# Kernel optimization log

Hardware: AMD Instinct MI355X
Metric: run time of the kernel (lower is better)

## Reference

```python
import jax, jax.numpy as jnp
import numpy as np

B, C_IN, C_OUT, H, W, W_DIM, K = 4, 64, 64, 512, 512, 512, 3
LRELU_SLOPE = 0.2
ACT_GAIN = np.sqrt(2.0).astype(np.float32)  # lrelu def_gain
CONV_CLAMP = 256.0


def setup_inputs() -> dict:
    key = jax.random.key(0)
    ks = jax.random.split(key, 5)
    return {
        "x": jax.random.normal(ks[0], (B, C_IN, H, W), dtype=jnp.float32),
        "ws": jax.random.normal(ks[1], (B, W_DIM), dtype=jnp.float32),
        "noise": jax.random.normal(ks[2], (B, 1, H, W), dtype=jnp.float32),
        "affine_weight": jax.random.normal(ks[3], (C_IN, W_DIM), dtype=jnp.float32),
        "affine_bias": jnp.ones((C_IN,), dtype=jnp.float32),
        "conv_weight": jax.random.normal(ks[4], (C_OUT, C_IN, K, K), dtype=jnp.float32),
        "bias": jnp.zeros((C_OUT,), dtype=jnp.float32),
    }


def reference(x, ws, noise, affine_weight, affine_bias, conv_weight, bias):
    b, c_in, h, w_sp = x.shape
    c_out, _, kh, kw = conv_weight.shape
    w_dim = ws.shape[1]

    # Affine (FullyConnectedLayer with equalized LR: weight_gain = 1/sqrt(w_dim), bias_init=1)
    styles = ws @ (affine_weight.T * np.float32(1.0 / np.sqrt(w_dim))) + affine_bias  # [b, c_in]

    # Modulate per-sample weights: w = weight[None] * styles
    wmod = conv_weight[None] * styles[:, None, :, None, None]  # [b, c_out, c_in, kh, kw]

    # Demodulation coefficients
    demod = jax.lax.rsqrt(jnp.sum(jnp.square(wmod), axis=(2, 3, 4)) + 1e-8)  # [b, c_out]
    wmod = wmod * demod[:, :, None, None, None]

    # Fused grouped conv: groups = batch (conv2d_resample, up=down=1, flip_weight=True -> correlation)
    xg = x.reshape(1, b * c_in, h, w_sp)
    wg = wmod.reshape(b * c_out, c_in, kh, kw)
    pad = kh // 2
    y = jax.lax.conv_general_dilated(
        xg, wg, window_strides=(1, 1), padding=[(pad, pad), (pad, pad)],
        dimension_numbers=("NCHW", "OIHW", "NCHW"), feature_group_count=b)
    y = y.reshape(b, c_out, h, w_sp)

    # Noise add (broadcast over channels)
    y = y + noise

    # bias_act: bias + lrelu * act_gain, then clamp (conv_clamp * gain, gain=1)
    y = y + bias[None, :, None, None]
    y = jnp.where(y >= 0, y, LRELU_SLOPE * y) * ACT_GAIN
    y = jnp.clip(y, -CONV_CLAMP, CONV_CLAMP)
    return y
```

## Files before the change

kernel.cpp:

```cpp
#include <hip/hip_runtime.h>
#include <math.h>

#define HH 512
#define WW 512
#define HW (HH * WW)
#define PW 514
#define PPIX (PW * PW)

typedef short bf16x8 __attribute__((ext_vector_type(8)));
typedef float f32x4 __attribute__((ext_vector_type(4)));

__device__ __forceinline__ ushort f2bf(float f) {
    union { float f; uint u; } c; c.f = f;
    uint u = c.u;
    return (ushort)((u + 0x7fffu + ((u >> 16) & 1u)) >> 16);
}

__device__ __forceinline__ uint cvtpk(float a, float b) {
    uint r;
    asm("v_cvt_pk_bf16_f32 %0, %1, %2" : "=v"(r) : "v"(a), "v"(b));
    return r;
}

__global__ void k_styles(const float* __restrict__ wsv, const float* __restrict__ aw,
                         const float* __restrict__ ab, float* __restrict__ styles) {
    int bid = blockIdx.x;
    int b = bid >> 6, ci = bid & 63;
    int l = threadIdx.x;
    const float* wrow = wsv + b * 512;
    const float* arow = aw + ci * 512;
    float s = 0.f;
    #pragma unroll
    for (int j = 0; j < 8; ++j)
        s += wrow[l + 64 * j] * arow[l + 64 * j];
    #pragma unroll
    for (int off = 32; off; off >>= 1)
        s += __shfl_xor(s, off, 64);
    if (l == 0)
        styles[b * 64 + ci] = s * 0.044194173824159216f + ab[ci];
}

__global__ void k_wmod(const float* __restrict__ cw, const float* __restrict__ styles,
                       ushort* __restrict__ wb) {
    int b = blockIdx.x >> 6, co = blockIdx.x & 63;
    int ci = threadIdx.x;
    float st = styles[b * 64 + ci];
    const float* wp = cw + (co * 64 + ci) * 9;
    float wv[9];
    float ss = 0.f;
    #pragma unroll
    for (int k = 0; k < 9; ++k) { wv[k] = wp[k] * st; ss += wv[k] * wv[k]; }
    #pragma unroll
    for (int off = 32; off; off >>= 1)
        ss += __shfl_xor(ss, off, 64);
    float dm = 1.0f / sqrtf(ss + 1e-8f);
    int cisw = ((((ci >> 3) ^ co) & 7) << 3) | (ci & 7);
    #pragma unroll
    for (int k = 0; k < 9; ++k)
        wb[((size_t)(b * 64 + co) * 9 + k) * 64 + cisw] = f2bf(wv[k] * dm);
}

__global__ void k_zeropad(ushort* __restrict__ xp) {
    int id = blockIdx.x * 256 + threadIdx.x;
    if (id >= 4 * 2052) return;
    int b = id / 2052, r = id % 2052;
    int gyp, gxp;
    if (r < 514)       { gyp = 0;        gxp = r; }
    else if (r < 1028) { gyp = 513;      gxp = r - 514; }
    else if (r < 1540) { gyp = r - 1027; gxp = 0; }
    else               { gyp = r - 1539; gxp = 513; }
    ushort* p = xp + (((size_t)b * PW + gyp) * PW + gxp) * 64;
    uint4 z = make_uint4(0, 0, 0, 0);
    #pragma unroll
    for (int i = 0; i < 8; ++i) *(uint4*)(p + i * 8) = z;
}

__global__ __launch_bounds__(256) void k_xpose(
    const float* __restrict__ x, ushort* __restrict__ xp) {
    __shared__ ushort lt[128 * 68];
    const int t = threadIdx.x;
    const int bid = blockIdx.x;
    const int gxt = bid & 3;
    const int gy  = (bid >> 2) & 511;
    const int b   = bid >> 11;

    const float* xb = x + (size_t)b * 64 * HW + (size_t)gy * WW + gxt * 128;
    const int ci0 = 8 * (t >> 5);
    const int gxc = t & 31;

    f32x4 v[8];
    #pragma unroll
    for (int j = 0; j < 8; ++j)
        v[j] = *(const f32x4*)(xb + (size_t)(ci0 + j) * HW + gxc * 4);

    #pragma unroll
    for (int p = 0; p < 4; ++p) {
        int px = gxc * 4 + p;
        int rowp = ((px & 3) * 32 + (px >> 2)) * 68;
        #pragma unroll
        for (int cg = 0; cg < 2; ++cg) {
            uint lo = cvtpk(v[4 * cg + 0][p], v[4 * cg + 1][p]);
            uint hi = cvtpk(v[4 * cg + 2][p], v[4 * cg + 3][p]);
            *(uint2*)&lt[rowp + ci0 + 4 * cg] = make_uint2(lo, hi);
        }
    }
    __syncthreads();

    const int px = t >> 1, half = t & 1;
    const int rowp = ((px & 3) * 32 + (px >> 2)) * 68 + half * 32;
    uint4 o0 = *(uint4*)&lt[rowp + 0];
    uint4 o1 = *(uint4*)&lt[rowp + 8];
    uint4 o2 = *(uint4*)&lt[rowp + 16];
    uint4 o3 = *(uint4*)&lt[rowp + 24];
    ushort* dst = xp + (((size_t)b * PW + (gy + 1)) * PW + (gxt * 128 + px + 1)) * 64
                     + half * 32;
    *(uint4*)(dst + 0)  = o0;
    *(uint4*)(dst + 8)  = o1;
    *(uint4*)(dst + 16) = o2;
    *(uint4*)(dst + 24) = o3;
}

__global__ __launch_bounds__(256) void k_conv(
    const ushort* __restrict__ xp,
    const ushort* __restrict__ wb,
    const float* __restrict__ noise,
    const float* __restrict__ bias,
    float* __restrict__ out) {
    __shared__ ushort tileB[1472 * 8];
    __shared__ ushort wlds[32 * 9 * 64];

    const int t = threadIdx.x;
    const int b = blockIdx.y;
    const int coh = blockIdx.z;
    const int colb = blockIdx.x & 31;
    const int rowb = blockIdx.x >> 5;
    const int tx = colb * 16, ty = rowb * 8;
    const int w = t >> 6;
    const int lane = t & 63;

    const ushort* xpb = xp + (size_t)b * PPIX * 64;
    const ushort* wA  = wb + (size_t)(b * 64 + coh * 32) * 576;

    for (int j = w; j < 36; j += 4) {
        const ushort* src = wA + j * 512 + lane * 8;
        __builtin_amdgcn_global_load_lds(
            (const __attribute__((address_space(1))) unsigned int*)src,
            (__attribute__((address_space(3))) unsigned int*)&wlds[j * 512],
            16, 0, 0);
    }
    for (int j = w; j < 23; j += 4) {
        int c = j * 64 + lane;
        int c2 = c < 1439 ? c : 1439;
        int cig = c2 & 7;
        int pxl = c2 >> 3;
        int row = pxl / 18;
        int lcol = pxl - row * 18;
        int gsrc = cig ^ (lcol & 7);
        const ushort* src = xpb + ((size_t)(ty + row) * PW + (tx + lcol)) * 64 + gsrc * 8;
        __builtin_amdgcn_global_load_lds(
            (const __attribute__((address_space(1))) unsigned int*)src,
            (__attribute__((address_space(3))) unsigned int*)&tileB[j * 512],
            16, 0, 0);
    }
    asm volatile("s_waitcnt vmcnt(0)" ::: "memory");
    __syncthreads();

    const int lr = lane & 15;
    const int lq = lane >> 4;

    int aidx[2][2];
    #pragma unroll
    for (int mt = 0; mt < 2; ++mt)
        #pragma unroll
        for (int kb = 0; kb < 2; ++kb)
            aidx[mt][kb] = (mt * 16 + lr) * 576 + ((((kb << 2) | lq) ^ (lr & 7)) << 3);

    int bidx[2][3];
    #pragma unroll
    for (int i = 0; i < 2; ++i)
        #pragma unroll
        for (int dx = 0; dx < 3; ++dx) {
            int lcol = lr + dx;
            bidx[i][dx] = ((2 * w + i) * 18 + lcol) * 64 + ((lq * 8) ^ ((lcol & 7) << 3));
        }

    f32x4 acc[2][2];
    #pragma unroll
    for (int mt = 0; mt < 2; ++mt)
        #pragma unroll
        for (int i = 0; i < 2; ++i) acc[mt][i] = (f32x4){0.f, 0.f, 0.f, 0.f};

    #pragma unroll
    for (int dy = 0; dy < 3; ++dy) {
        #pragma unroll
        for (int dx = 0; dx < 3; ++dx) {
            #pragma unroll
            for (int kb = 0; kb < 2; ++kb) {
                const int off = dy * 3 + dx;
                bf16x8 afr[2], bfr[2];
                #pragma unroll
                for (int mt = 0; mt < 2; ++mt)
                    afr[mt] = *(const bf16x8*)&wlds[aidx[mt][kb] + off * 64];
                #pragma unroll
                for (int i = 0; i < 2; ++i) {
                    int idx = (bidx[i][dx] + dy * (18 * 64)) ^ (kb << 5);
                    bfr[i] = *(const bf16x8*)&tileB[idx];
                }
                #pragma unroll
                for (int mt = 0; mt < 2; ++mt)
                    #pragma unroll
                    for (int i = 0; i < 2; ++i)
                        acc[mt][i] = __builtin_amdgcn_mfma_f32_16x16x32_bf16(
                            afr[mt], bfr[i], acc[mt][i], 0, 0, 0);
            }
        }
    }

    const float* nz = noise + (size_t)b * HW;
    float nv[2];
    int gyv[2];
    const int gx = tx + lr;
    #pragma unroll
    for (int i = 0; i < 2; ++i) {
        gyv[i] = ty + 2 * w + i;
        nv[i] = nz[gyv[i] * WW + gx];
    }
    #pragma unroll
    for (int mt = 0; mt < 2; ++mt) {
        f32x4 bv = *(const f32x4*)&bias[coh * 32 + mt * 16 + lq * 4];
        #pragma unroll
        for (int i = 0; i < 2; ++i) {
            #pragma unroll
            for (int rg2 = 0; rg2 < 4; ++rg2) {
                int co = coh * 32 + mt * 16 + lq * 4 + rg2;
                float y = acc[mt][i][rg2] + nv[i] + bv[rg2];
                y = (y >= 0.f ? y : 0.2f * y) * 1.41421356237f;
                y = fminf(fmaxf(y, -256.f), 256.f);
                out[((size_t)(b * 64 + co) * HH + gyv[i]) * WW + gx] = y;
            }
        }
    }
}

extern "C" void kernel_launch(void* const* d_in, const int* in_sizes, int n_in,
                              void* d_out, int out_size, void* d_ws, size_t ws_size,
                              hipStream_t stream) {
    const float* x     = (const float*)d_in[0];
    const float* wsv   = (const float*)d_in[1];
    const float* noise = (const float*)d_in[2];
    const float* aw    = (const float*)d_in[3];
    const float* ab    = (const float*)d_in[4];
    const float* cw    = (const float*)d_in[5];
    const float* bias  = (const float*)d_in[6];
    float* out = (float*)d_out;

    float*  styles = (float*)d_ws;
    ushort* wb16   = (ushort*)((char*)d_ws + 1024);
    ushort* xpad   = (ushort*)((char*)d_ws + (1 << 20));

    k_styles<<<256, 64, 0, stream>>>(wsv, aw, ab, styles);
    k_wmod<<<256, 64, 0, stream>>>(cw, styles, wb16);
    k_zeropad<<<33, 256, 0, stream>>>(xpad);
    k_xpose<<<8192, 256, 0, stream>>>(x, xpad);
    dim3 grid(2048, 4, 2);
    k_conv<<<grid, 256, 0, stream>>>(xpad, wb16, noise, bias, out);
}
```

Baseline: 267.9 us.

## Make conv kernel persistent over 16 tiles with double-buffered input staging

The conv kernel now launches 512 blocks. Each block loads all 64 output channels' modulated weights into LDS once and loops over 16 spatial tiles. The next input tile is prefetched into a second LDS buffer with async global-to-LDS loads while the current tile is computed. Each wave now covers all four 16-channel groups, so every loaded input fragment is reused across twice as many channels. The intent is to remove the repeated weight reloads and the half-channel input duplication, and to hide the input load latency. In exchange it uses more LDS (about 120 KB) and more accumulator registers, which lowers occupancy, and it leaves only 512 blocks to spread across the CUs.

Result: no change. 267.5 us (-0.2%).

```diff
diff --git a/kernel.cpp b/kernel.cpp
--- a/kernel.cpp
+++ b/kernel.cpp
@@ -6,6 +6,10 @@
 #define HW (HH * WW)
 #define PW 514
 #define PPIX (PW * PW)
+
+#define A_U    36864
+#define B_STR  12032
+#define LDS_BYTES ((A_U + 2 * B_STR) * 2)
 
 typedef short bf16x8 __attribute__((ext_vector_type(8)));
 typedef float f32x4 __attribute__((ext_vector_type(4)));
@@ -120,34 +124,10 @@
     *(uint4*)(dst + 24) = o3;
 }
 
-__global__ __launch_bounds__(256) void k_conv(
-    const ushort* __restrict__ xp,
-    const ushort* __restrict__ wb,
-    const float* __restrict__ noise,
-    const float* __restrict__ bias,
-    float* __restrict__ out) {
-    __shared__ ushort tileB[1472 * 8];
-    __shared__ ushort wlds[32 * 9 * 64];
-
-    const int t = threadIdx.x;
-    const int b = blockIdx.y;
-    const int coh = blockIdx.z;
-    const int colb = blockIdx.x & 31;
-    const int rowb = blockIdx.x >> 5;
-    const int tx = colb * 16, ty = rowb * 8;
-    const int w = t >> 6;
-    const int lane = t & 63;
-
-    const ushort* xpb = xp + (size_t)b * PPIX * 64;
-    const ushort* wA  = wb + (size_t)(b * 64 + coh * 32) * 576;
-
-    for (int j = w; j < 36; j += 4) {
-        const ushort* src = wA + j * 512 + lane * 8;
-        __builtin_amdgcn_global_load_lds(
-            (const __attribute__((address_space(1))) unsigned int*)src,
-            (__attribute__((address_space(3))) unsigned int*)&wlds[j * 512],
-            16, 0, 0);
-    }
+__device__ __forceinline__ void stage_b(ushort* lds, const ushort* __restrict__ xpb,
+                                        int p, int tidx, int w, int lane) {
+    const int ty = (tidx >> 5) * 8;
+    const int tx = (tidx & 31) * 16;
     for (int j = w; j < 23; j += 4) {
         int c = j * 64 + lane;
         int c2 = c < 1439 ? c : 1439;
@@ -159,21 +139,49 @@
         const ushort* src = xpb + ((size_t)(ty + row) * PW + (tx + lcol)) * 64 + gsrc * 8;
         __builtin_amdgcn_global_load_lds(
             (const __attribute__((address_space(1))) unsigned int*)src,
-            (__attribute__((address_space(3))) unsigned int*)&tileB[j * 512],
+            (__attribute__((address_space(3))) unsigned int*)&lds[A_U + p * B_STR + j * 512],
             16, 0, 0);
     }
+}
+
+__global__ __launch_bounds__(256) void k_conv(
+    const ushort* __restrict__ xp,
+    const ushort* __restrict__ wb,
+    const float* __restrict__ noise,
+    const float* __restrict__ bias,
+    float* __restrict__ out) {
+    extern __shared__ __align__(16) ushort lds[];
+
+    const int t = threadIdx.x;
+    const int w = t >> 6;
+    const int lane = t & 63;
+    const int blk = blockIdx.x;
+    const int b = blk >> 7;
+    const int tile0 = (blk & 127) * 16;
+
+    const ushort* xpb = xp + (size_t)b * PPIX * 64;
+    const ushort* wA  = wb + (size_t)b * 64 * 576;
+
+    for (int j = w; j < 72; j += 4) {
+        const ushort* src = wA + j * 512 + lane * 8;
+        __builtin_amdgcn_global_load_lds(
+            (const __attribute__((address_space(1))) unsigned int*)src,
+            (__attribute__((address_space(3))) unsigned int*)&lds[j * 512],
+            16, 0, 0);
+    }
+    stage_b(lds, xpb, 0, tile0, w, lane);
     asm volatile("s_waitcnt vmcnt(0)" ::: "memory");
     __syncthreads();
 
     const int lr = lane & 15;
     const int lq = lane >> 4;
 
-    int aidx[2][2];
-    #pragma unroll
-    for (int mt = 0; mt < 2; ++mt)
+    int aidx[4][2];
+    #pragma unroll
+    for (int m = 0; m < 4; ++m)
         #pragma unroll
         for (int kb = 0; kb < 2; ++kb)
-            aidx[mt][kb] = (mt * 16 + lr) * 576 + ((((kb << 2) | lq) ^ (lr & 7)) << 3);
+            aidx[m][kb] = (m * 16 + lr) * 576 + ((((kb << 2) | lq) ^ (lr & 7)) << 3);
 
     int bidx[2][3];
     #pragma unroll
@@ -184,61 +192,80 @@
             bidx[i][dx] = ((2 * w + i) * 18 + lcol) * 64 + ((lq * 8) ^ ((lcol & 7) << 3));
         }
 
-    f32x4 acc[2][2];
-    #pragma unroll
-    for (int mt = 0; mt < 2; ++mt)
-        #pragma unroll
-        for (int i = 0; i < 2; ++i) acc[mt][i] = (f32x4){0.f, 0.f, 0.f, 0.f};
-
-    #pragma unroll
-    for (int dy = 0; dy < 3; ++dy) {
-        #pragma unroll
-        for (int dx = 0; dx < 3; ++dx) {
+    f32x4 bv[4];
+    #pragma unroll
+    for (int m = 0; m < 4; ++m)
+        bv[m] = *(const f32x4*)&bias[m * 16 + lq * 4];
+    const float* nz = noise + (size_t)b * HW;
+
+    int p = 0;
+    for (int it = 0; it < 16; ++it) {
+        const int tidx = tile0 + it;
+        const int ty = (tidx >> 5) * 8;
+        const int tx = (tidx & 31) * 16;
+        const int gx = tx + lr;
+
+        if (it < 15) stage_b(lds, xpb, p ^ 1, tidx + 1, w, lane);
+
+        float nv[2];
+        int gyv[2];
+        #pragma unroll
+        for (int i = 0; i < 2; ++i) {
+            gyv[i] = ty + 2 * w + i;
+            nv[i] = nz[gyv[i] * WW + gx];
+        }
+
+        const ushort* bufp = &lds[A_U + p * B_STR];
+        f32x4 acc[4][2];
+        #pragma unroll
+        for (int m = 0; m < 4; ++m)
             #pragma unroll
-            for (int kb = 0; kb < 2; ++kb) {
-                const int off = dy * 3 + dx;
-                bf16x8 afr[2], bfr[2];
+            for (int i = 0; i < 2; ++i) acc[m][i] = (f32x4){0.f, 0.f, 0.f, 0.f};
+
+        #pragma unroll
+        for (int dy = 0; dy < 3; ++dy) {
+            #pragma unroll
+            for (int dx = 0; dx < 3; ++dx) {
                 #pragma unroll
-                for (int mt = 0; mt < 2; ++mt)
-                    afr[mt] = *(const bf16x8*)&wlds[aidx[mt][kb] + off * 64];
+                for (int kb = 0; kb < 2; ++kb) {
+                    const int off = dy * 3 + dx;
+                    bf16x8 afr[4], bfr[2];
+                    #pragma unroll
+                    for (int m = 0; m < 4; ++m)
+                        afr[m] = *(const bf16x8*)&lds[aidx[m][kb] + off * 64];
+                    #pragma unroll
+                    for (int i = 0; i < 2; ++i) {
+                        int idx = (bidx[i][dx] + dy * (18 * 64)) ^ (kb << 5);
+                        bfr[i] = *(const bf16x8*)&bufp[idx];
+                    }
+                    #pragma unroll
+                    for (int m = 0; m < 4; ++m)
+                        #pragma unroll
+                        for (int i = 0; i < 2; ++i)
+                            acc[m][i] = __builtin_amdgcn_mfma_f32_16x16x32_bf16(
+                                afr[m], bfr[i], acc[m][i], 0, 0, 0);
+                }
+            }
+        }
+
+        asm volatile("s_waitcnt vmcnt(0)" ::: "memory");
+        __syncthreads();
+
+        #pragma unroll
+        for (int m = 0; m < 4; ++m) {
+            #pragma unroll
+            for (int i = 0; i < 2; ++i) {
                 #pragma unroll
-                for (int i = 0; i < 2; ++i) {
-                    int idx = (bidx[i][dx] + dy * (18 * 64)) ^ (kb << 5);
-                    bfr[i] = *(const bf16x8*)&tileB[idx];
+                for (int rg2 = 0; rg2 < 4; ++rg2) {
+                    int co = m * 16 + lq * 4 + rg2;
+                    float y = acc[m][i][rg2] + nv[i] + bv[m][rg2];
+                    y = (y >= 0.f ? y : 0.2f * y) * 1.41421356237f;
+                    y = fminf(fmaxf(y, -256.f), 256.f);
+                    out[((size_t)(b * 64 + co) * HH + gyv[i]) * WW + gx] = y;
                 }
-                #pragma unroll
-                for (int mt = 0; mt < 2; ++mt)
-                    #pragma unroll
-                    for (int i = 0; i < 2; ++i)
-                        acc[mt][i] = __builtin_amdgcn_mfma_f32_16x16x32_bf16(
-                            afr[mt], bfr[i], acc[mt][i], 0, 0, 0);
             }
         }
-    }
-
-    const float* nz = noise + (size_t)b * HW;
-    float nv[2];
-    int gyv[2];
-    const int gx = tx + lr;
-    #pragma unroll
-    for (int i = 0; i < 2; ++i) {
-        gyv[i] = ty + 2 * w + i;
-        nv[i] = nz[gyv[i] * WW + gx];
-    }
-    #pragma unroll
-    for (int mt = 0; mt < 2; ++mt) {
-        f32x4 bv = *(const f32x4*)&bias[coh * 32 + mt * 16 + lq * 4];
-        #pragma unroll
-        for (int i = 0; i < 2; ++i) {
-            #pragma unroll
-            for (int rg2 = 0; rg2 < 4; ++rg2) {
-                int co = coh * 32 + mt * 16 + lq * 4 + rg2;
-                float y = acc[mt][i][rg2] + nv[i] + bv[rg2];
-                y = (y >= 0.f ? y : 0.2f * y) * 1.41421356237f;
-                y = fminf(fmaxf(y, -256.f), 256.f);
-                out[((size_t)(b * 64 + co) * HH + gyv[i]) * WW + gx] = y;
-            }
-        }
+        p ^= 1;
     }
 }
 
@@ -258,10 +285,12 @@
     ushort* wb16   = (ushort*)((char*)d_ws + 1024);
     ushort* xpad   = (ushort*)((char*)d_ws + (1 << 20));
 
+    hipFuncSetAttribute((const void*)k_conv,
+                        hipFuncAttributeMaxDynamicSharedMemorySize, LDS_BYTES);
+
     k_styles<<<256, 64, 0, stream>>>(wsv, aw, ab, styles);
     k_wmod<<<256, 64, 0, stream>>>(cw, styles, wb16);
     k_zeropad<<<33, 256, 0, stream>>>(xpad);
     k_xpose<<<8192, 256, 0, stream>>>(x, xpad);
-    dim3 grid(2048, 4, 2);
-    k_conv<<<grid, 256, 0, stream>>>(xpad, wb16, noise, bias, out);
-}
+    k_conv<<<512, 256, LDS_BYTES, stream>>>(xpad, wb16, noise, bias, out);
+}
```
